# Kernel tuning notes

Measured on AMD Instinct MI355X. Metric: run time of the kernel, lower is better.

The kernel has to match this reference:

```python
import jax, jax.numpy as jnp
import numpy as np

B = 4096; CPG = 2; NPC = 25              # graphs, components/graph, nodes/component
N = B * CPG * NPC; C = B * CPG; E = 409600
IN_CH = 128; HID = 256; L = 3; S = 64; M = 8; NCLS = 2
BN_EPS = 1e-5

def _leaky(x):
    return jax.nn.leaky_relu(x, 0.01)

def _gin_conv(x, src, dst, wa, ba, wb, bb):
    # GINConv with eps=0: mlp(x + sum_{j in N(i)} x_j); messages flow src->dst
    agg = jnp.zeros_like(x).at[dst].add(x[src])
    h = x + agg
    return jax.nn.relu(h @ wa + ba) @ wb + bb

def setup_inputs():
    key = jax.random.key(0)
    ks = jax.random.split(key, 12)
    rn = lambda k, shp: jax.random.normal(k, shp, jnp.float32) * 0.05
    return {
        "x": jax.random.normal(ks[0], (N, IN_CH), jnp.float32),
        "w0a": rn(ks[1], (IN_CH, HID)), "b0a": jnp.zeros((HID,), jnp.float32),
        "w0b": rn(ks[2], (HID, HID)), "b0b": jnp.zeros((HID,), jnp.float32),
        "wra": rn(ks[3], (L - 1, HID, HID)), "bra": jnp.zeros((L - 1, HID), jnp.float32),
        "wrb": rn(ks[4], (L - 1, HID, HID)), "brb": jnp.zeros((L - 1, HID), jnp.float32),
        "Wc": jax.random.uniform(ks[5], (HID, S * M), jnp.float32, -1.0, 1.0),
        "fc1_w": rn(ks[6], (S, 32)), "fc1_b": jnp.zeros((32,), jnp.float32),
        "bn_g": jnp.ones((32,), jnp.float32), "bn_b": jnp.zeros((32,), jnp.float32),
        "fc2_w": rn(ks[7], (32, NCLS)), "fc2_b": jnp.zeros((NCLS,), jnp.float32),
        "edge_index": jax.random.randint(ks[8], (2, E), 0, N, jnp.int32),
        "node2comp": (jnp.arange(N, dtype=jnp.int32) // NPC),
        "comp2graph": (jnp.arange(C, dtype=jnp.int32) // CPG),
        "comp_pos": (jnp.arange(C, dtype=jnp.int32) % CPG),
        "n_graphs": B,
        "max_comps": CPG,
    }

def reference(x, w0a, b0a, w0b, b0b, wra, bra, wrb, brb, Wc, fc1_w, fc1_b, bn_g, bn_b, fc2_w, fc2_b, edge_index, node2comp, comp2graph, comp_pos, n_graphs, max_comps):
    src, dst = edge_index[0], edge_index[1]
    # --- GIN backbone (num_layers convs, ReLU between layers) ---
    h = _gin_conv(x, src, dst, w0a, b0a, w0b, b0b)
    for i in range(wra.shape[0]):
        h = jax.nn.relu(h)
        h = _gin_conv(h, src, dst, wra[i], bra[i], wrb[i], brb[i])
    # --- per-connected-component mean pooling ---
    n_comp = comp2graph.shape[0]
    comp_sum = jax.ops.segment_sum(h, node2comp, num_segments=n_comp)           # [C, d]
    comp_size = jax.ops.segment_sum(jnp.ones((h.shape[0],), h.dtype), node2comp, num_segments=n_comp)
    # torch.mean over the zero-padded cardinality dim divides by the per-graph MAX component size
    graph_maxc = jax.ops.segment_max(comp_size, comp2graph, num_segments=n_graphs)
    comp_mean = comp_sum / graph_maxc[comp2graph][:, None]
    # --- pad components into [B, max_comps, d] ---
    X = jnp.zeros((n_graphs, max_comps, h.shape[1]), h.dtype).at[comp2graph, comp_pos].set(comp_mean)
    # --- set-rep classifier ---
    t = _leaky(jnp.einsum('bcd,dk->bck', X, Wc))                                # [B, maxC, S*M]
    s = fc1_w.shape[0]; m = Wc.shape[1] // s
    t = t.reshape(t.shape[0], t.shape[1], m, s)                                 # view(B, maxC, n_elements, n_hidden_sets)
    t = jnp.max(t, axis=2)
    t = jnp.sum(t, axis=1)                                                      # [B, S]
    t = t @ fc1_w + fc1_b
    mu = jnp.mean(t, axis=0); var = jnp.var(t, axis=0)                          # BN, batch stats (track_running_stats=False)
    t = (t - mu) / jnp.sqrt(var + BN_EPS) * bn_g + bn_b
    t = _leaky(t)
    out = t @ fc2_w + fc2_b
    return jax.nn.log_softmax(out, axis=1)
```

## Files before the change

### kernel.cpp

```cpp
#include <hip/hip_runtime.h>
#include <hip/hip_fp16.h>
#include <math.h>

typedef unsigned short u16;
typedef float f32x4 __attribute__((ext_vector_type(4)));
typedef __bf16 bf16x8 __attribute__((ext_vector_type(8)));

__device__ __forceinline__ float b2f(u16 u) {
    union { unsigned int i; float f; } v; v.i = ((unsigned int)u) << 16; return v.f;
}
__device__ __forceinline__ u16 f2b(float f) {
    union { float f; unsigned int i; } v; v.f = f;
    unsigned int lsb = (v.i >> 16) & 1u;
    return (u16)((v.i + 0x7fffu + lsb) >> 16);
}

__global__ __launch_bounds__(256)
void k_count(const int* __restrict__ dst, int* __restrict__ cnt, int E)
{
    int e = blockIdx.x * 256 + threadIdx.x;
    if (e < E) atomicAdd(&cnt[dst[e]], 1);
}

__global__ __launch_bounds__(256)
void k_scan1(const int* __restrict__ cnt, int* __restrict__ rowptr,
             int* __restrict__ bsum, int N)
{
    __shared__ int s[256];
    int t = threadIdx.x, i = blockIdx.x * 256 + t;
    int v = (i < N) ? cnt[i] : 0;
    s[t] = v;
    __syncthreads();
#pragma unroll
    for (int off = 1; off < 256; off <<= 1) {
        int add = (t >= off) ? s[t - off] : 0;
        __syncthreads();
        s[t] += add;
        __syncthreads();
    }
    if (i < N) rowptr[i] = s[t] - v;
    if (t == 255) bsum[blockIdx.x] = s[255];
}

__global__ __launch_bounds__(256)
void k_scan2(const int* __restrict__ bsum, int* __restrict__ bscan, int nb)
{
    __shared__ int s[256];
    int t = threadIdx.x;
    int g[4], e[4];
    int base = t * 4;
#pragma unroll
    for (int j = 0; j < 4; ++j) g[j] = (base + j < nb) ? bsum[base + j] : 0;
    e[0] = 0; e[1] = g[0]; e[2] = g[0] + g[1]; e[3] = g[0] + g[1] + g[2];
    int tsum = e[3] + g[3];
    s[t] = tsum;
    __syncthreads();
#pragma unroll
    for (int off = 1; off < 256; off <<= 1) {
        int add = (t >= off) ? s[t - off] : 0;
        __syncthreads();
        s[t] += add;
        __syncthreads();
    }
    int texcl = s[t] - tsum;
#pragma unroll
    for (int j = 0; j < 4; ++j)
        if (base + j < nb) bscan[base + j] = texcl + e[j];
}

__global__ __launch_bounds__(256)
void k_scan3(int* __restrict__ rowptr, const int* __restrict__ bscan,
             int* __restrict__ cursor, int N)
{
    int i = blockIdx.x * 256 + threadIdx.x;
    if (i >= N) return;
    int r = rowptr[i] + bscan[i >> 8];
    rowptr[i] = r;
    cursor[i] = r;
}

__global__ __launch_bounds__(256)
void k_fill(const int* __restrict__ src, const int* __restrict__ dst,
            int* __restrict__ cursor, int* __restrict__ col, int E)
{
    int e = blockIdx.x * 256 + threadIdx.x;
    if (e >= E) return;
    int pos = atomicAdd(&cursor[dst[e]], 1);
    col[pos] = src[e];
}

__global__ void k_T(const float* __restrict__ in, u16* __restrict__ out, int K, int N)
{
    int t = blockIdx.x * 256 + threadIdx.x;
    if (t >= K * N) return;
    int n = t / K, k = t % K;
    out[t] = f2b(in[k * N + n]);
}

template<int K, bool RELU, bool F32SRC>
__global__ __launch_bounds__(256, 4)
void k_gin(const void* __restrict__ hsrc,
           const int* __restrict__ cnt, const int* __restrict__ rowptr,
           const int* __restrict__ col,
           const u16* __restrict__ WaT, const float* __restrict__ ba,
           const u16* __restrict__ WbT, const float* __restrict__ bb,
           u16* __restrict__ Hout)
{
    __shared__ u16 AH[64 * 256];

    const int tid = threadIdx.x, lane = tid & 63, wave = tid >> 6;
    const int bm0 = blockIdx.x * 64;
    const int lc = lane & 15, lr = (lane >> 4) * 4;
    const int cw0 = wave * 64;
    const int l15 = lane & 15, lq = lane >> 4;

    {
        const int r    = tid >> 2;
        const int seg  = tid & 3;
        const int node = bm0 + r;
        const int nn = cnt[node], rp = rowptr[node];
        constexpr int KSEG = K / 4;
        constexpr int NP   = KSEG / 32;
        u16* const wbase = AH + (r >> 4) * 512 + (r & 15) * 8;
#pragma unroll
        for (int p = 0; p < NP; ++p) {
            const int k0 = seg * KSEG + p * 32;
            float acc[32];
#pragma unroll
            for (int i = 0; i < 32; ++i) acc[i] = 0.f;
            for (int j = -1; j < nn; ++j) {
                const int sIdx = (j < 0) ? node : col[rp + j];
                if (F32SRC) {
                    const float4* q = (const float4*)((const float*)hsrc + (size_t)sIdx * K + k0);
#pragma unroll
                    for (int cc = 0; cc < 8; ++cc) {
                        float4 v = q[cc];
                        if (RELU) {
                            v.x = fmaxf(v.x, 0.f); v.y = fmaxf(v.y, 0.f);
                            v.z = fmaxf(v.z, 0.f); v.w = fmaxf(v.w, 0.f);
                        }
                        acc[cc * 4 + 0] += v.x; acc[cc * 4 + 1] += v.y;
                        acc[cc * 4 + 2] += v.z; acc[cc * 4 + 3] += v.w;
                    }
                } else {
                    const uint4* q = (const uint4*)((const u16*)hsrc + (size_t)sIdx * K + k0);
#pragma unroll
                    for (int cc = 0; cc < 4; ++cc) {
                        u16 vs[8] __attribute__((aligned(16)));
                        *(uint4*)vs = q[cc];
#pragma unroll
                        for (int i2 = 0; i2 < 8; ++i2) {
                            float x = b2f(vs[i2]);
                            acc[cc * 8 + i2] += RELU ? fmaxf(x, 0.f) : x;
                        }
                    }
                }
            }
            u16* wp = wbase + (k0 >> 5) * 2048;
#pragma unroll
            for (int kc = 0; kc < 4; ++kc) {
                u16 tmp[8] __attribute__((aligned(16)));
#pragma unroll
                for (int jj = 0; jj < 8; ++jj) tmp[jj] = f2b(acc[kc * 8 + jj]);
                *(uint4*)(wp + kc * 128) = *(const uint4*)tmp;
            }
        }
    }
    __syncthreads();

    constexpr int NK1 = K / 32;
    f32x4 acc1[4][4];
#pragma unroll
    for (int r = 0; r < 4; ++r)
#pragma unroll
        for (int c = 0; c < 4; ++c) acc1[r][c] = (f32x4){0.f, 0.f, 0.f, 0.f};

#pragma unroll
    for (int kb = 0; kb < NK1; ++kb) {
        bf16x8 a[4], b[4];
#pragma unroll
        for (int c = 0; c < 4; ++c)
            b[c] = *(const bf16x8*)(WaT + (size_t)(cw0 + c * 16 + l15) * K + kb * 32 + lq * 8);
#pragma unroll
        for (int r = 0; r < 4; ++r)
            a[r] = *(const bf16x8*)&AH[(kb * 256 + r * 64 + lane) * 8];
        __builtin_amdgcn_s_setprio(1);
#pragma unroll
        for (int r = 0; r < 4; ++r)
#pragma unroll
            for (int c = 0; c < 4; ++c)
                acc1[r][c] = __builtin_amdgcn_mfma_f32_16x16x32_bf16(a[r], b[c], acc1[r][c], 0, 0, 0);
        __builtin_amdgcn_s_setprio(0);
    }
    __syncthreads();

#pragma unroll
    for (int c = 0; c < 4; ++c) {
        const int n = cw0 + c * 16 + lc;
        const float bv = ba[n];
        const int nb = (n >> 5) * 256 + ((n >> 3) & 3) * 16;
#pragma unroll
        for (int r = 0; r < 4; ++r)
#pragma unroll
            for (int i = 0; i < 4; ++i)
                AH[(nb + r * 64 + lr + i) * 8 + (n & 7)] = f2b(fmaxf(acc1[r][c][i] + bv, 0.f));
    }
    __syncthreads();

    f32x4 acc2[4][4];
#pragma unroll
    for (int r = 0; r < 4; ++r)
#pragma unroll
        for (int c = 0; c < 4; ++c) acc2[r][c] = (f32x4){0.f, 0.f, 0.f, 0.f};

#pragma unroll
    for (int kb = 0; kb < 8; ++kb) {
        bf16x8 a[4], b[4];
#pragma unroll
        for (int c = 0; c < 4; ++c)
            b[c] = *(const bf16x8*)(WbT + (size_t)(cw0 + c * 16 + l15) * 256 + kb * 32 + lq * 8);
#pragma unroll
        for (int r = 0; r < 4; ++r)
            a[r] = *(const bf16x8*)&AH[(kb * 256 + r * 64 + lane) * 8];
        __builtin_amdgcn_s_setprio(1);
#pragma unroll
        for (int r = 0; r < 4; ++r)
#pragma unroll
            for (int c = 0; c < 4; ++c)
                acc2[r][c] = __builtin_amdgcn_mfma_f32_16x16x32_bf16(a[r], b[c], acc2[r][c], 0, 0, 0);
        __builtin_amdgcn_s_setprio(0);
    }
#pragma unroll
    for (int c = 0; c < 4; ++c) {
        const int n = cw0 + c * 16 + lc;
        const float bv = bb[n];
#pragma unroll
        for (int r = 0; r < 4; ++r)
#pragma unroll
            for (int i = 0; i < 4; ++i)
                Hout[(size_t)(bm0 + r * 16 + lr + i) * 256 + n] = f2b(acc2[r][c][i] + bv);
    }
}

__global__ __launch_bounds__(256)
void k_lin(const u16* __restrict__ A, const u16* __restrict__ WT,
           float* __restrict__ C)
{
    __shared__ u16 As[64 * 40];
    __shared__ u16 Bs[256 * 40];
    const int tid = threadIdx.x, lane = tid & 63, wave = tid >> 6;
    const int bm0 = blockIdx.x * 64, bn0 = blockIdx.y * 256;
    const int fm = lane & 15, fk = (lane >> 4) * 8;
    const int lc = lane & 15, lr = (lane >> 4) * 4;
    const int cw0 = wave * 64;
    const int sr = tid >> 2, sc = tid & 3;

    f32x4 acc[4][4];
#pragma unroll
    for (int r = 0; r < 4; ++r)
#pragma unroll
        for (int c = 0; c < 4; ++c) acc[r][c] = (f32x4){0.f, 0.f, 0.f, 0.f};

    for (int k0 = 0; k0 < 256; k0 += 32) {
        *(uint4*)&As[sr * 40 + sc * 8] =
            *(const uint4*)(A + (size_t)(bm0 + sr) * 256 + k0 + sc * 8);
        {
            const uint4* wp = (const uint4*)(WT + (size_t)(bn0 + tid) * 256 + k0);
#pragma unroll
            for (int c = 0; c < 4; ++c)
                *(uint4*)&Bs[tid * 40 + c * 8] = wp[c];
        }
        __syncthreads();
        bf16x8 a[4], b[4];
#pragma unroll
        for (int r = 0; r < 4; ++r) a[r] = *(const bf16x8*)&As[(r * 16 + fm) * 40 + fk];
#pragma unroll
        for (int c = 0; c < 4; ++c) b[c] = *(const bf16x8*)&Bs[(cw0 + c * 16 + fm) * 40 + fk];
#pragma unroll
        for (int r = 0; r < 4; ++r)
#pragma unroll
            for (int c = 0; c < 4; ++c)
                acc[r][c] = __builtin_amdgcn_mfma_f32_16x16x32_bf16(a[r], b[c], acc[r][c], 0, 0, 0);
        __syncthreads();
    }
#pragma unroll
    for (int c = 0; c < 4; ++c) {
        const int col = bn0 + cw0 + c * 16 + lc;
#pragma unroll
        for (int r = 0; r < 4; ++r)
#pragma unroll
            for (int i = 0; i < 4; ++i) {
                float v = acc[r][c][i];
                v = (v >= 0.f) ? v : 0.01f * v;
                C[(size_t)(bm0 + r * 16 + lr + i) * 512 + col] = v;
            }
    }
}

__global__ void k_pool(const u16* __restrict__ H, u16* __restrict__ Xc)
{
    int c = blockIdx.x, f = threadIdx.x;
    const u16* p = H + (size_t)c * 25 * 256 + f;
    float s = 0.f;
#pragma unroll
    for (int j = 0; j < 25; ++j) s += b2f(p[j * 256]);
    Xc[(size_t)c * 256 + f] = f2b(s / 25.0f);
}

__global__ void k_setpool(const float* __restrict__ T, float* __restrict__ Tp)
{
    int tid = blockIdx.x * 256 + threadIdx.x;
    int b = tid >> 6, s = tid & 63;
    float acc = 0.f;
#pragma unroll
    for (int c = 0; c < 2; ++c) {
        const float* row = T + ((size_t)(b * 2 + c)) * 512 + s;
        float mx = row[0];
#pragma unroll
        for (int m = 1; m < 8; ++m) mx = fmaxf(mx, row[m * 64]);
        acc += mx;
    }
    Tp[tid] = acc;
}

__global__ void k_fc1(const float* __restrict__ Tp, const float* __restrict__ w,
                      const float* __restrict__ b, float* __restrict__ T1)
{
    int tid = blockIdx.x * 256 + threadIdx.x;
    int bb = tid >> 5, j = tid & 31;
    float s = b[j];
#pragma unroll
    for (int k = 0; k < 64; ++k) s += Tp[bb * 64 + k] * w[k * 32 + j];
    T1[tid] = s;
}

__global__ void k_bnstats(const float* __restrict__ T1, float* __restrict__ stats)
{
    __shared__ float r1[256], r2[256];
    const int j = blockIdx.x, t = threadIdx.x;
    float s = 0.f, ss = 0.f;
    for (int b = t; b < 4096; b += 256) {
        float v = T1[b * 32 + j];
        s += v; ss += v * v;
    }
    r1[t] = s; r2[t] = ss;
    __syncthreads();
    for (int off = 128; off > 0; off >>= 1) {
        if (t < off) { r1[t] += r1[t + off]; r2[t] += r2[t + off]; }
        __syncthreads();
    }
    if (t == 0) {
        float mu  = r1[0] * (1.f / 4096.f);
        float var = r2[0] * (1.f / 4096.f) - mu * mu;
        stats[j]      = mu;
        stats[32 + j] = 1.f / sqrtf(var + 1e-5f);
    }
}

__global__ void k_head(const float* __restrict__ T1, const float* __restrict__ stats,
                       const float* __restrict__ g, const float* __restrict__ bb,
                       const float* __restrict__ w2, const float* __restrict__ b2,
                       float* __restrict__ out)
{
    const int b = blockIdx.x * 256 + threadIdx.x;
    float l0 = b2[0], l1 = b2[1];
#pragma unroll
    for (int j = 0; j < 32; ++j) {
        float v = (T1[b * 32 + j] - stats[j]) * stats[32 + j] * g[j] + bb[j];
        v = (v >= 0.f) ? v : 0.01f * v;
        l0 += v * w2[j * 2];
        l1 += v * w2[j * 2 + 1];
    }
    float mx  = fmaxf(l0, l1);
    float lse = mx + logf(expf(l0 - mx) + expf(l1 - mx));
    out[b * 2]     = l0 - lse;
    out[b * 2 + 1] = l1 - lse;
}

extern "C" void kernel_launch(void* const* d_in, const int* in_sizes, int n_in,
                              void* d_out, int out_size, void* d_ws, size_t ws_size,
                              hipStream_t stream)
{
    (void)n_in; (void)out_size; (void)ws_size;
    constexpr int NN = 204800, NCOMP = 8192, NGRAPH = 4096;

    const float* x    = (const float*)d_in[0];
    const float* w0a  = (const float*)d_in[1];
    const float* b0a  = (const float*)d_in[2];
    const float* w0b  = (const float*)d_in[3];
    const float* b0b  = (const float*)d_in[4];
    const float* wra  = (const float*)d_in[5];
    const float* bra  = (const float*)d_in[6];
    const float* wrb  = (const float*)d_in[7];
    const float* brb  = (const float*)d_in[8];
    const float* Wc   = (const float*)d_in[9];
    const float* f1w  = (const float*)d_in[10];
    const float* f1b  = (const float*)d_in[11];
    const float* bng  = (const float*)d_in[12];
    const float* bnb  = (const float*)d_in[13];
    const float* f2w  = (const float*)d_in[14];
    const float* f2bb = (const float*)d_in[15];
    const int* ei   = (const int*)d_in[16];
    const int  E    = in_sizes[16] / 2;
    const int* src  = ei;
    const int* dst  = ei + E;

    char* ws = (char*)d_ws;
    u16*    H1  = (u16*)ws;
    u16*    H0  = (u16*)(ws + (size_t)104857600);
    u16*    wt  = (u16*)(ws + (size_t)209715200);
    u16 *WT0 = wt, *WT1 = wt + 65536, *WT2 = wt + 131072, *WT3 = wt + 196608,
        *WT4 = wt + 262144, *WT5 = wt + 327680, *WT6 = wt + 393216;
    char* csr = ws + (size_t)210763776;
    int* cnt    = (int*)csr;
    int* rowptr = (int*)(csr + 819200);
    int* cursor = (int*)(csr + 1638400);
    int* col    = (int*)(csr + 2457600);
    int* bsum   = (int*)(csr + 4096000);
    int* bscan  = (int*)(csr + 4100096);
    u16*   Xc    = (u16*)ws;
    float* Tfull = (float*)(ws + (size_t)16777216);
    float* Tp    = (float*)(ws + (size_t)33554432);
    float* T1    = (float*)(ws + (size_t)41943040);
    float* stats = (float*)(ws + (size_t)46137344);

    const dim3 blk(256);
    const int NB = NN / 256;

    hipMemsetAsync(cnt, 0, NN * 4, stream);
    k_count<<<(E + 255) / 256, blk, 0, stream>>>(dst, cnt, E);
    k_scan1<<<NB, blk, 0, stream>>>(cnt, rowptr, bsum, NN);
    k_scan2<<<1, blk, 0, stream>>>(bsum, bscan, NB);
    k_scan3<<<NB, blk, 0, stream>>>(rowptr, bscan, cursor, NN);
    k_fill<<<(E + 255) / 256, blk, 0, stream>>>(src, dst, cursor, col, E);

    k_T<<<128, blk, 0, stream>>>(w0a, WT0, 128, 256);
    k_T<<<256, blk, 0, stream>>>(w0b, WT1, 256, 256);
    k_T<<<256, blk, 0, stream>>>(wra,          WT2, 256, 256);
    k_T<<<256, blk, 0, stream>>>(wra + 65536,  WT3, 256, 256);
    k_T<<<256, blk, 0, stream>>>(wrb,          WT4, 256, 256);
    k_T<<<256, blk, 0, stream>>>(wrb + 65536,  WT5, 256, 256);
    k_T<<<512, blk, 0, stream>>>(Wc, WT6, 256, 512);

    k_gin<128, false, true><<<NN / 64, blk, 0, stream>>>(
        x, cnt, rowptr, col, WT0, b0a, WT1, b0b, H0);
    k_gin<256, true, false><<<NN / 64, blk, 0, stream>>>(
        H0, cnt, rowptr, col, WT2, bra, WT4, brb, H1);
    k_gin<256, true, false><<<NN / 64, blk, 0, stream>>>(
        H1, cnt, rowptr, col, WT3, bra + 256, WT5, brb + 256, H0);

    k_pool<<<NCOMP, blk, 0, stream>>>(H0, Xc);
    k_lin<<<dim3(NCOMP / 64, 2), blk, 0, stream>>>(Xc, WT6, Tfull);
    k_setpool<<<(NGRAPH * 64) / 256, blk, 0, stream>>>(Tfull, Tp);
    k_fc1<<<(NGRAPH * 32) / 256, blk, 0, stream>>>(Tp, f1w, f1b, T1);
    k_bnstats<<<32, blk, 0, stream>>>(T1, stats);
    k_head<<<NGRAPH / 256, blk, 0, stream>>>(T1, stats, bng, bnb, f2w, f2bb, (float*)d_out);
}
```

Baseline: 804.9 us.

## Halve GIN block rows, stage neighbor indices in LDS, prefetch gathers

Each fused GIN block now covers 32 nodes instead of 64, which doubles the grid and raises the occupancy hint to 5 blocks per CU. The block's CSR column indices are first copied into shared memory. Eight threads per node now gather one contiguous feature segment each, and the next neighbor's row is loaded before the current one is accumulated. The goal is more parallelism and latency hiding in the gather-bound aggregation. In exchange, the weight tiles are reloaded twice as often per node and each wave issues fewer MFMAs per weight load.

```diff
diff --git a/kernel.cpp b/kernel.cpp
--- a/kernel.cpp
+++ b/kernel.cpp
@@ -97,96 +97,126 @@
     out[t] = f2b(in[k * N + n]);
 }
 
+#define CCAP 512
+
 template<int K, bool RELU, bool F32SRC>
-__global__ __launch_bounds__(256, 4)
+__global__ __launch_bounds__(256, 5)
 void k_gin(const void* __restrict__ hsrc,
            const int* __restrict__ cnt, const int* __restrict__ rowptr,
            const int* __restrict__ col,
            const u16* __restrict__ WaT, const float* __restrict__ ba,
            const u16* __restrict__ WbT, const float* __restrict__ bb,
-           u16* __restrict__ Hout)
-{
-    __shared__ u16 AH[64 * 256];
+           u16* __restrict__ Hout, int Ntot, int Etot)
+{
+    __shared__ u16 AH[32 * 256];
+    __shared__ int colLDS[CCAP];
 
     const int tid = threadIdx.x, lane = tid & 63, wave = tid >> 6;
-    const int bm0 = blockIdx.x * 64;
+    const int bm0 = blockIdx.x * 32;
     const int lc = lane & 15, lr = (lane >> 4) * 4;
     const int cw0 = wave * 64;
     const int l15 = lane & 15, lq = lane >> 4;
 
+    const int rp0 = rowptr[bm0];
+    const int rpE = (bm0 + 32 < Ntot) ? rowptr[bm0 + 32] : Etot;
+    const int total = rpE - rp0;
+    for (int i = tid; i < total && i < CCAP; i += 256) colLDS[i] = col[rp0 + i];
+    __syncthreads();
+
     {
-        const int r    = tid >> 2;
-        const int seg  = tid & 3;
-        const int node = bm0 + r;
+        constexpr int NSEG = K / 8;
+        const int gr = tid >> 3, gseg = tid & 7;
+        const int node = bm0 + gr;
         const int nn = cnt[node], rp = rowptr[node];
-        constexpr int KSEG = K / 4;
-        constexpr int NP   = KSEG / 32;
-        u16* const wbase = AH + (r >> 4) * 512 + (r & 15) * 8;
-#pragma unroll
-        for (int p = 0; p < NP; ++p) {
-            const int k0 = seg * KSEG + p * 32;
-            float acc[32];
-#pragma unroll
-            for (int i = 0; i < 32; ++i) acc[i] = 0.f;
-            for (int j = -1; j < nn; ++j) {
-                const int sIdx = (j < 0) ? node : col[rp + j];
-                if (F32SRC) {
-                    const float4* q = (const float4*)((const float*)hsrc + (size_t)sIdx * K + k0);
-#pragma unroll
-                    for (int cc = 0; cc < 8; ++cc) {
-                        float4 v = q[cc];
-                        if (RELU) {
-                            v.x = fmaxf(v.x, 0.f); v.y = fmaxf(v.y, 0.f);
-                            v.z = fmaxf(v.z, 0.f); v.w = fmaxf(v.w, 0.f);
-                        }
-                        acc[cc * 4 + 0] += v.x; acc[cc * 4 + 1] += v.y;
-                        acc[cc * 4 + 2] += v.z; acc[cc * 4 + 3] += v.w;
-                    }
+        const int jbase = rp - rp0;
+        const int nIt = nn + 1;
+
+        float acc[NSEG];
+#pragma unroll
+        for (int i = 0; i < NSEG; ++i) acc[i] = 0.f;
+
+        if (F32SRC) {
+            const float4* bp = (const float4*)hsrc;
+            const int stride = K / 4, off = gseg * (NSEG / 4);
+            const float4* p = bp + (size_t)node * stride + off;
+            float4 a0 = p[0], a1 = p[1];
+            for (int t = 0; t < nIt; ++t) {
+                float4 b0 = p[2], b1 = p[3];
+                int tn = (t + 1 < nIt) ? t + 1 : t;
+                int jl = jbase + tn - 1;
+                int idxN = (tn == 0) ? node : ((jl < CCAP) ? colLDS[jl] : col[rp + tn - 1]);
+                const float4* q = bp + (size_t)idxN * stride + off;
+                float4 n0 = q[0], n1 = q[1];
+                if (RELU) {
+                    acc[0] += fmaxf(a0.x,0.f); acc[1] += fmaxf(a0.y,0.f); acc[2] += fmaxf(a0.z,0.f); acc[3] += fmaxf(a0.w,0.f);
+                    acc[4] += fmaxf(a1.x,0.f); acc[5] += fmaxf(a1.y,0.f); acc[6] += fmaxf(a1.z,0.f); acc[7] += fmaxf(a1.w,0.f);
+                    acc[8] += fmaxf(b0.x,0.f); acc[9] += fmaxf(b0.y,0.f); acc[10]+= fmaxf(b0.z,0.f); acc[11]+= fmaxf(b0.w,0.f);
+                    acc[12]+= fmaxf(b1.x,0.f); acc[13]+= fmaxf(b1.y,0.f); acc[14]+= fmaxf(b1.z,0.f); acc[15]+= fmaxf(b1.w,0.f);
                 } else {
-                    const uint4* q = (const uint4*)((const u16*)hsrc + (size_t)sIdx * K + k0);
-#pragma unroll
-                    for (int cc = 0; cc < 4; ++cc) {
-                        u16 vs[8] __attribute__((aligned(16)));
-                        *(uint4*)vs = q[cc];
-#pragma unroll
-                        for (int i2 = 0; i2 < 8; ++i2) {
-                            float x = b2f(vs[i2]);
-                            acc[cc * 8 + i2] += RELU ? fmaxf(x, 0.f) : x;
-                        }
-                    }
+                    acc[0] += a0.x; acc[1] += a0.y; acc[2] += a0.z; acc[3] += a0.w;
+                    acc[4] += a1.x; acc[5] += a1.y; acc[6] += a1.z; acc[7] += a1.w;
+                    acc[8] += b0.x; acc[9] += b0.y; acc[10]+= b0.z; acc[11]+= b0.w;
+                    acc[12]+= b1.x; acc[13]+= b1.y; acc[14]+= b1.z; acc[15]+= b1.w;
                 }
+                a0 = n0; a1 = n1; p = q;
             }
-            u16* wp = wbase + (k0 >> 5) * 2048;
-#pragma unroll
-            for (int kc = 0; kc < 4; ++kc) {
-                u16 tmp[8] __attribute__((aligned(16)));
-#pragma unroll
-                for (int jj = 0; jj < 8; ++jj) tmp[jj] = f2b(acc[kc * 8 + jj]);
-                *(uint4*)(wp + kc * 128) = *(const uint4*)tmp;
+        } else {
+            const uint4* bp = (const uint4*)hsrc;
+            const int stride = K / 8, off = gseg * (NSEG / 8);
+            const uint4* p = bp + (size_t)node * stride + off;
+            uint4 a0 = p[0], a1 = p[1];
+            for (int t = 0; t < nIt; ++t) {
+                uint4 b0 = p[2], b1 = p[3];
+                int tn = (t + 1 < nIt) ? t + 1 : t;
+                int jl = jbase + tn - 1;
+                int idxN = (tn == 0) ? node : ((jl < CCAP) ? colLDS[jl] : col[rp + tn - 1]);
+                const uint4* q = bp + (size_t)idxN * stride + off;
+                uint4 n0 = q[0], n1 = q[1];
+                u16 vs[32] __attribute__((aligned(16)));
+                *(uint4*)(vs + 0)  = a0; *(uint4*)(vs + 8)  = a1;
+                *(uint4*)(vs + 16) = b0; *(uint4*)(vs + 24) = b1;
+#pragma unroll
+                for (int i2 = 0; i2 < 32; ++i2) {
+                    float x = b2f(vs[i2]);
+                    acc[i2] += RELU ? fmaxf(x, 0.f) : x;
+                }
+                a0 = n0; a1 = n1; p = q;
             }
         }
+
+        const int k0 = gseg * NSEG;
+        u16* wp = AH + (gr >> 4) * 512 + (gr & 15) * 8 + (k0 >> 5) * 1024;
+        constexpr int NKC = NSEG / 8;
+        const int kcb = (k0 >> 3) & 3;
+#pragma unroll
+        for (int kcl = 0; kcl < NKC; ++kcl) {
+            u16 tmp[8] __attribute__((aligned(16)));
+#pragma unroll
+            for (int jj = 0; jj < 8; ++jj) tmp[jj] = f2b(acc[kcl * 8 + jj]);
+            *(uint4*)(wp + (kcb + kcl) * 128) = *(const uint4*)tmp;
+        }
     }
     __syncthreads();
 
     constexpr int NK1 = K / 32;
-    f32x4 acc1[4][4];
-#pragma unroll
-    for (int r = 0; r < 4; ++r)
+    f32x4 acc1[2][4];
+#pragma unroll
+    for (int r = 0; r < 2; ++r)
 #pragma unroll
         for (int c = 0; c < 4; ++c) acc1[r][c] = (f32x4){0.f, 0.f, 0.f, 0.f};
 
 #pragma unroll
     for (int kb = 0; kb < NK1; ++kb) {
-        bf16x8 a[4], b[4];
+        bf16x8 a[2], b[4];
 #pragma unroll
         for (int c = 0; c < 4; ++c)
             b[c] = *(const bf16x8*)(WaT + (size_t)(cw0 + c * 16 + l15) * K + kb * 32 + lq * 8);
 #pragma unroll
-        for (int r = 0; r < 4; ++r)
-            a[r] = *(const bf16x8*)&AH[(kb * 256 + r * 64 + lane) * 8];
+        for (int r = 0; r < 2; ++r)
+            a[r] = *(const bf16x8*)&AH[(kb * 128 + r * 64 + lane) * 8];
         __builtin_amdgcn_s_setprio(1);
 #pragma unroll
-        for (int r = 0; r < 4; ++r)
+        for (int r = 0; r < 2; ++r)
 #pragma unroll
             for (int c = 0; c < 4; ++c)
                 acc1[r][c] = __builtin_amdgcn_mfma_f32_16x16x32_bf16(a[r], b[c], acc1[r][c], 0, 0, 0);
@@ -198,33 +228,33 @@
     for (int c = 0; c < 4; ++c) {
         const int n = cw0 + c * 16 + lc;
         const float bv = ba[n];
-        const int nb = (n >> 5) * 256 + ((n >> 3) & 3) * 16;
-#pragma unroll
-        for (int r = 0; r < 4; ++r)
+        const int nb = (n >> 5) * 128 + ((n >> 3) & 3) * 16;
+#pragma unroll
+        for (int r = 0; r < 2; ++r)
 #pragma unroll
             for (int i = 0; i < 4; ++i)
                 AH[(nb + r * 64 + lr + i) * 8 + (n & 7)] = f2b(fmaxf(acc1[r][c][i] + bv, 0.f));
     }
     __syncthreads();
 
-    f32x4 acc2[4][4];
-#pragma unroll
-    for (int r = 0; r < 4; ++r)
+    f32x4 acc2[2][4];
+#pragma unroll
+    for (int r = 0; r < 2; ++r)
 #pragma unroll
         for (int c = 0; c < 4; ++c) acc2[r][c] = (f32x4){0.f, 0.f, 0.f, 0.f};
 
 #pragma unroll
     for (int kb = 0; kb < 8; ++kb) {
-        bf16x8 a[4], b[4];
+        bf16x8 a[2], b[4];
 #pragma unroll
         for (int c = 0; c < 4; ++c)
             b[c] = *(const bf16x8*)(WbT + (size_t)(cw0 + c * 16 + l15) * 256 + kb * 32 + lq * 8);
 #pragma unroll
-        for (int r = 0; r < 4; ++r)
-            a[r] = *(const bf16x8*)&AH[(kb * 256 + r * 64 + lane) * 8];
+        for (int r = 0; r < 2; ++r)
+            a[r] = *(const bf16x8*)&AH[(kb * 128 + r * 64 + lane) * 8];
         __builtin_amdgcn_s_setprio(1);
 #pragma unroll
-        for (int r = 0; r < 4; ++r)
+        for (int r = 0; r < 2; ++r)
 #pragma unroll
             for (int c = 0; c < 4; ++c)
                 acc2[r][c] = __builtin_amdgcn_mfma_f32_16x16x32_bf16(a[r], b[c], acc2[r][c], 0, 0, 0);
@@ -235,7 +265,7 @@
         const int n = cw0 + c * 16 + lc;
         const float bv = bb[n];
 #pragma unroll
-        for (int r = 0; r < 4; ++r)
+        for (int r = 0; r < 2; ++r)
 #pragma unroll
             for (int i = 0; i < 4; ++i)
                 Hout[(size_t)(bm0 + r * 16 + lr + i) * 256 + n] = f2b(acc2[r][c][i] + bv);
@@ -442,12 +472,12 @@
     k_T<<<256, blk, 0, stream>>>(wrb + 65536,  WT5, 256, 256);
     k_T<<<512, blk, 0, stream>>>(Wc, WT6, 256, 512);
 
-    k_gin<128, false, true><<<NN / 64, blk, 0, stream>>>(
-        x, cnt, rowptr, col, WT0, b0a, WT1, b0b, H0);
-    k_gin<256, true, false><<<NN / 64, blk, 0, stream>>>(
-        H0, cnt, rowptr, col, WT2, bra, WT4, brb, H1);
-    k_gin<256, true, false><<<NN / 64, blk, 0, stream>>>(
-        H1, cnt, rowptr, col, WT3, bra + 256, WT5, brb + 256, H0);
+    k_gin<128, false, true><<<NN / 32, blk, 0, stream>>>(
+        x, cnt, rowptr, col, WT0, b0a, WT1, b0b, H0, NN, E);
+    k_gin<256, true, false><<<NN / 32, blk, 0, stream>>>(
+        H0, cnt, rowptr, col, WT2, bra, WT4, brb, H1, NN, E);
+    k_gin<256, true, false><<<NN / 32, blk, 0, stream>>>(
+        H1, cnt, rowptr, col, WT3, bra + 256, WT5, brb + 256, H0, NN, E);
 
     k_pool<<<NCOMP, blk, 0, stream>>>(H0, Xc);
     k_lin<<<dim3(NCOMP / 64, 2), blk, 0, stream>>>(Xc, WT6, Tfull);
```

New measurement: 909.5 us. +13.0%, slower.
